# Kernel tuning notes

Measured on AMD Instinct MI355X. Metric: run time of the kernel, lower is better.

## Reference

```python
import jax, jax.numpy as jnp
import numpy as np

B, T, F = 8192, 336, 8
H = 20        # lstm_hidden_size
DENSE = 20
OUT = 1
N_LAYERS = 3


def _param(key, shape, scale):
    return jax.random.uniform(key, shape, jnp.float32, -scale, scale)


def setup_inputs() -> dict:
    key = jax.random.key(0)
    ks = jax.random.split(key, 32)
    s = 1.0 / np.sqrt(H)
    inp = {"x": jax.random.normal(ks[0], (B, T, F), jnp.float32)}
    k = 1
    for l in range(N_LAYERS):
        in_size = F if l == 0 else H
        inp[f"W_ih{l}"] = _param(ks[k], (4 * H, in_size), s); k += 1
        inp[f"W_hh{l}"] = _param(ks[k], (4 * H, H), s); k += 1
        inp[f"b_ih{l}"] = _param(ks[k], (4 * H,), s); k += 1
        inp[f"b_hh{l}"] = _param(ks[k], (4 * H,), s); k += 1
    inp["fc1_w"] = _param(ks[k], (DENSE, H), 1.0 / np.sqrt(H)); k += 1
    inp["fc1_b"] = _param(ks[k], (DENSE,), 1.0 / np.sqrt(H)); k += 1
    inp["fc2_w"] = _param(ks[k], (OUT, DENSE), 1.0 / np.sqrt(DENSE)); k += 1
    inp["fc2_b"] = _param(ks[k], (OUT,), 1.0 / np.sqrt(DENSE)); k += 1
    return inp


def lstm_layer(x, W_ih, W_hh, b_ih, b_hh):
    """PyTorch-convention LSTM over [B, T, in]; returns hidden sequence [B, T, H]."""
    b = x.shape[0]
    # Precompute input contribution for all timesteps in one GEMM: [B, T, 4H]
    xg = jnp.einsum('bti,gi->btg', x, W_ih) + b_ih + b_hh
    W_hh_T = W_hh.T  # [H, 4H]

    def step(carry, xt):
        h, c = carry
        gates = xt + h @ W_hh_T                      # [B, 4H], gate order i,f,g,o
        i, f, g, o = jnp.split(gates, 4, axis=-1)
        i = jax.nn.sigmoid(i)
        f = jax.nn.sigmoid(f)
        g = jnp.tanh(g)
        o = jax.nn.sigmoid(o)
        c = f * c + i * g
        h = o * jnp.tanh(c)
        return (h, c), h

    h0 = jnp.zeros((b, W_hh.shape[1]), x.dtype)
    c0 = jnp.zeros_like(h0)
    _, hs = jax.lax.scan(step, (h0, c0), jnp.swapaxes(xg, 0, 1))  # [T, B, H]
    return jnp.swapaxes(hs, 0, 1)


def reference(x, W_ih0, W_hh0, b_ih0, b_hh0, W_ih1, W_hh1, b_ih1, b_hh1,
              W_ih2, W_hh2, b_ih2, b_hh2, fc1_w, fc1_b, fc2_w, fc2_b):
    layers = [(W_ih0, W_hh0, b_ih0, b_hh0),
              (W_ih1, W_hh1, b_ih1, b_hh1),
              (W_ih2, W_hh2, b_ih2, b_hh2)]
    h = x
    for (wi, wh, bi, bh) in layers:
        h = lstm_layer(h, wi, wh, bi, bh)
    h = h[:, -1, :]                         # last timestep, [B, H]
    # dropout layers are identity at inference
    h = jax.nn.relu(h @ fc1_w.T + fc1_b)    # [B, DENSE]
    return h @ fc2_w.T + fc2_b              # [B, OUT]
```

## Files before the change

### kernel.cpp

```cpp
#include <hip/hip_runtime.h>


#define T_LEN 336
#define NJ 85

typedef _Float16 f16;
typedef _Float16 f16x4 __attribute__((ext_vector_type(4)));
typedef _Float16 f16x8 __attribute__((ext_vector_type(8)));
typedef float f32x4 __attribute__((ext_vector_type(4)));
typedef int i32x2 __attribute__((ext_vector_type(2)));
typedef int i32x4 __attribute__((ext_vector_type(4)));

#define MFMA(a, b, c) __builtin_amdgcn_mfma_f32_16x16x32_f16((a), (b), (c), 0, 0, 0)

#define SWZ1(n, c) ((c) ^ (((n) & 7) << 3))

#define KS1 1.4426950408889634f
#define KS2 2.8853900817779268f

__device__ __forceinline__ float sigm_p(float y) {
  return __builtin_amdgcn_rcpf(1.0f + __builtin_amdgcn_exp2f(y));
}
__device__ __forceinline__ float tanh_p(float y) {
  return 2.0f * __builtin_amdgcn_rcpf(1.0f + __builtin_amdgcn_exp2f(y)) - 1.0f;
}
__device__ __forceinline__ float tanh_fast(float x) {
  return 2.0f * __builtin_amdgcn_rcpf(1.0f + __builtin_amdgcn_exp2f(-KS2 * x)) - 1.0f;
}

#define CELLS5(DI, DF, DG, DO, DL, HV, HL) {                                                \
  { float i_=sigm_p((DI)[0]), f_=sigm_p((DF)[0]), g_=tanh_p((DG)[0]), o_=sigm_p((DO)[0]);   \
    c0 = f_*c0 + i_*g_; (HV)[0] = (f16)(o_*tanh_fast(c0)); }                                \
  { float i_=sigm_p((DI)[1]), f_=sigm_p((DF)[1]), g_=tanh_p((DG)[1]), o_=sigm_p((DO)[1]);   \
    c1 = f_*c1 + i_*g_; (HV)[1] = (f16)(o_*tanh_fast(c1)); }                                \
  { float i_=sigm_p((DI)[2]), f_=sigm_p((DF)[2]), g_=tanh_p((DG)[2]), o_=sigm_p((DO)[2]);   \
    c2 = f_*c2 + i_*g_; (HV)[2] = (f16)(o_*tanh_fast(c2)); }                                \
  { float i_=sigm_p((DI)[3]), f_=sigm_p((DF)[3]), g_=tanh_p((DG)[3]), o_=sigm_p((DO)[3]);   \
    c3 = f_*c3 + i_*g_; (HV)[3] = (f16)(o_*tanh_fast(c3)); }                                \
  { float i_=sigm_p((DL)[0]), f_=sigm_p((DL)[1]), g_=tanh_p((DL)[2]), o_=sigm_p((DL)[3]);   \
    cL = f_*cL + i_*g_; (HL) = (f16)(o_*tanh_fast(cL)); } }

#define MSTEP_REG(BA, PUB) {                                                                \
  i32x2 _lo = __builtin_bit_cast(i32x2, hvS);                                               \
  int _hlu = (int)(unsigned)__builtin_bit_cast(unsigned short, hlS);                        \
  int _b0 = __builtin_amdgcn_ds_bpermute(adrA, _lo.x);                                      \
  int _b1 = __builtin_amdgcn_ds_bpermute(adrA, _lo.y);                                      \
  int _b2 = __builtin_amdgcn_ds_bpermute(adrB, _lo.x);                                      \
  int _b3 = __builtin_amdgcn_ds_bpermute(adrB, _lo.y);                                      \
  int _hA = __builtin_amdgcn_ds_bpermute(adr0, _hlu);                                       \
  int _hB = __builtin_amdgcn_ds_bpermute(adr1, _hlu);                                       \
  int _hC = __builtin_amdgcn_ds_bpermute(adr2, _hlu);                                       \
  int _hD = __builtin_amdgcn_ds_bpermute(adr3, _hlu);                                       \
  int _w0 = (q < 2) ? _b0 : ((_hA & 0xffff) | (_hB << 16));                                 \
  int _w1 = (q < 2) ? _b1 : ((_hC & 0xffff) | (_hD << 16));                                 \
  i32x4 _bbi = { _w0, _w1, _b2, _b3 };                                                      \
  f16x8 bb = __builtin_bit_cast(f16x8, _bbi);                                               \
  f32x4 di = MFMA(Fb0, bb, MFMA(Fa0, (BA), Bi));                                            \
  f32x4 df = MFMA(Fb1, bb, MFMA(Fa1, (BA), Bf));                                            \
  f32x4 dg = MFMA(Fb2, bb, MFMA(Fa2, (BA), Bg));                                            \
  f32x4 dn = MFMA(Fb3, bb, MFMA(Fa3, (BA), Bo));                                            \
  f32x4 dl = MFMA(Fb4, bb, MFMA(Fa4, (BA), BL));                                            \
  f16x4 hv; f16 hl; CELLS5(di, df, dg, dn, dl, hv, hl)                                      \
  hvS = hv; hlS = hl;                                                                       \
  f16* dp_ = (PUB);                                                                         \
  if (dp_) { *(f16x4*)&dp_[n * 64 + SWZ1(n, q * 4)] = hv;                                   \
             dp_[n * 64 + SWZ1(n, 16 + q)] = hl; } }

#define L0S(S, D, PUB) {                                                                    \
  f16x8 b0 = *(const f16x8*)&zT0[S][n * 64 + SWZ1(n, q * 8)];                               \
  f32x4 di = MFMA(Fa0, b0, Bi), df = MFMA(Fa1, b0, Bf), dg = MFMA(Fa2, b0, Bg),             \
        dn = MFMA(Fa3, b0, Bo), dl = MFMA(Fa4, b0, BL);                                     \
  f16x4 hv; f16 hl; CELLS5(di, df, dg, dn, dl, hv, hl)                                      \
  *(f16x4*)&zT0[D][n * 64 + SWZ1(n, 8 + q * 4)] = hv;                                       \
  zT0[D][n * 64 + SWZ1(n, 24 + q)] = hl;                                                    \
  f16* dp_ = (PUB);                                                                         \
  *(f16x4*)&dp_[n * 64 + SWZ1(n, q * 4)] = hv;                                              \
  dp_[n * 64 + SWZ1(n, 16 + q)] = hl; }

__global__ __launch_bounds__(192, 2) void lstm3_ws_kernel(
    const float* __restrict__ x,
    const float* __restrict__ Wih0, const float* __restrict__ Whh0,
    const float* __restrict__ bih0, const float* __restrict__ bhh0,
    const float* __restrict__ Wih1, const float* __restrict__ Whh1,
    const float* __restrict__ bih1, const float* __restrict__ bhh1,
    const float* __restrict__ Wih2, const float* __restrict__ Whh2,
    const float* __restrict__ bih2, const float* __restrict__ bhh2,
    const float* __restrict__ fc1w, const float* __restrict__ fc1b,
    const float* __restrict__ fc2w, const float* __restrict__ fc2b,
    float* __restrict__ out)
{
  __shared__ __align__(16) f16 zT0[4][16 * 64];
  __shared__ __align__(16) f16 zT1[2][4][16 * 64];
  __shared__ __align__(16) f16 zT2[2][4][16 * 64];
  __shared__ __align__(16) float pbuf[64];

  const int tid  = threadIdx.x;
  const int w    = tid >> 6;
  const int lane = tid & 63;
  const int n = lane & 15;
  const int q = lane >> 4;

  const int adrA = 4 * (n + 32 * (q & 1));
  const int adrB = 4 * (n + 16 + 32 * (q & 1));
  const int adr0 = 4 * n, adr1 = 4 * (n + 16), adr2 = 4 * (n + 32), adr3 = 4 * (n + 48);

  {
    f16x8 zer;
#pragma unroll
    for (int j = 0; j < 8; ++j) zer[j] = (f16)0.f;
    for (int i = tid; i < 512; i += 192)  ((f16x8*)&zT0[0][0])[i] = zer;
    for (int i = tid; i < 1024; i += 192) ((f16x8*)&zT1[0][0][0])[i] = zer;
    for (int i = tid; i < 1024; i += 192) ((f16x8*)&zT2[0][0][0])[i] = zer;
  }
  __syncthreads();

  auto rowmap = [](int T, int m) { return T < 4 ? T * 20 + m : (m & 3) * 20 + 16 + (m >> 2); };
  auto gscale = [](int T, int m) {
    int g = (T < 4) ? T : (m & 3);
    return (g == 2) ? -KS2 : -KS1;
  };

  f16x8 Fa0{}, Fa1{}, Fa2{}, Fa3{}, Fa4{};
  f16x8 Fb0{}, Fb1{}, Fb2{}, Fb3{}, Fb4{};
  f32x4 Bi{}, Bf{}, Bg{}, Bo{}, BL{};
  float c0 = 0.f, c1 = 0.f, c2 = 0.f, c3 = 0.f, cL = 0.f;
  f16x4 hvS{};
  f16 hlS = (f16)0.f;

  if (w == 0) {
    auto gA0 = [&](int T) {
      int row = rowmap(T, n);
      float sc = gscale(T, n);
      f16x8 r;
#pragma unroll
      for (int j = 0; j < 8; ++j) {
        int k = q * 8 + j;
        float v = (k < 8) ? Wih0[row * 8 + k] : (k < 28 ? Whh0[row * 20 + k - 8] : 0.f);
        r[j] = (f16)(sc * v);
      }
      return r;
    };
    Fa0 = gA0(0); Fa1 = gA0(1); Fa2 = gA0(2); Fa3 = gA0(3); Fa4 = gA0(4);
    auto gB = [&](int T) {
      f32x4 r;
#pragma unroll
      for (int j = 0; j < 4; ++j) {
        int m = q * 4 + j;
        int row = rowmap(T, m);
        r[j] = gscale(T, m) * (bih0[row] + bhh0[row]);
      }
      return r;
    };
    Bi = gB(0); Bf = gB(1); Bg = gB(2); Bo = gB(3); BL = gB(4);
  } else {
    const float* Wi = (w == 1) ? Wih1 : Wih2;
    const float* Wh = (w == 1) ? Whh1 : Whh2;
    const float* bi = (w == 1) ? bih1 : bih2;
    const float* bh = (w == 1) ? bhh1 : bhh2;
    auto gA = [&](int T, int c) {
      int row = rowmap(T, n);
      float sc = gscale(T, n);
      const float* W = c ? Wh : Wi;
      f16x8 r;
#pragma unroll
      for (int j = 0; j < 8; ++j) {
        int k = q * 8 + j;
        r[j] = (f16)((k < 20) ? sc * W[row * 20 + k] : 0.f);
      }
      return r;
    };
    Fa0 = gA(0, 0); Fb0 = gA(0, 1);
    Fa1 = gA(1, 0); Fb1 = gA(1, 1);
    Fa2 = gA(2, 0); Fb2 = gA(2, 1);
    Fa3 = gA(3, 0); Fb3 = gA(3, 1);
    Fa4 = gA(4, 0); Fb4 = gA(4, 1);
    auto gB = [&](int T) {
      f32x4 r;
#pragma unroll
      for (int j = 0; j < 4; ++j) {
        int m = q * 4 + j;
        int row = rowmap(T, m);
        r[j] = gscale(T, m) * (bi[row] + bh[row]);
      }
      return r;
    };
    Bi = gB(0); Bf = gB(1); Bg = gB(2); Bo = gB(3); BL = gB(4);
  }

  const float* xb = x + (size_t)(blockIdx.x * 16 + n) * (T_LEN * 8) + 4 * q;
  f32x4 xA{}, xB{};
  if (w == 0) {
    xA = *(const f32x4*)(xb);
    xB = *(const f32x4*)(xb + 16);
  }

#pragma unroll 1
  for (int j = 0; j <= NJ; ++j) {
    asm volatile("" ::: "memory");
    __builtin_amdgcn_s_setprio(1);
    const int wp = j & 1, rp = wp ^ 1;
    if (w == 0) {
      if (j <= 83) {
        f16x4 xh;
        xh[0] = (f16)xA[0]; xh[1] = (f16)xA[1]; xh[2] = (f16)xA[2]; xh[3] = (f16)xA[3];
        *(f16x4*)&zT0[q >> 1][n * 64 + SWZ1(n, 4 * (q & 1))] = xh;
        xh[0] = (f16)xB[0]; xh[1] = (f16)xB[1]; xh[2] = (f16)xB[2]; xh[3] = (f16)xB[3];
        *(f16x4*)&zT0[2 + (q >> 1)][n * 64 + SWZ1(n, 4 * (q & 1))] = xh;
        int g = (j + 1 > 83) ? 83 : j + 1;
        xA = *(const f32x4*)(xb + (size_t)(2 * g) * 16);
        xB = *(const f32x4*)(xb + (size_t)(2 * g + 1) * 16);
        f16* p1 = &zT1[wp][0][0];
        L0S(0, 1, p1 + 0 * 1024)
        L0S(1, 2, p1 + 1 * 1024)
        L0S(2, 3, p1 + 2 * 1024)
        L0S(3, 0, p1 + 3 * 1024)
      }
    } else if (w == 1) {
      if (j >= 1 && j <= 84) {
        f16* s1 = &zT1[rp][0][0];
        f16x8 ba0 = *(const f16x8*)&s1[0 * 1024 + n * 64 + SWZ1(n, q * 8)];
        f16x8 ba1 = *(const f16x8*)&s1[1 * 1024 + n * 64 + SWZ1(n, q * 8)];
        f16x8 ba2 = *(const f16x8*)&s1[2 * 1024 + n * 64 + SWZ1(n, q * 8)];
        f16x8 ba3 = *(const f16x8*)&s1[3 * 1024 + n * 64 + SWZ1(n, q * 8)];
        f16* p2 = &zT2[wp][0][0];
        MSTEP_REG(ba0, p2 + 0 * 1024)
        MSTEP_REG(ba1, p2 + 1 * 1024)
        MSTEP_REG(ba2, p2 + 2 * 1024)
        MSTEP_REG(ba3, p2 + 3 * 1024)
      }
    } else {
      if (j >= 2) {
        f16* s2 = &zT2[rp][0][0];
        f16x8 ca0 = *(const f16x8*)&s2[0 * 1024 + n * 64 + SWZ1(n, q * 8)];
        f16x8 ca1 = *(const f16x8*)&s2[1 * 1024 + n * 64 + SWZ1(n, q * 8)];
        f16x8 ca2 = *(const f16x8*)&s2[2 * 1024 + n * 64 + SWZ1(n, q * 8)];
        f16x8 ca3 = *(const f16x8*)&s2[3 * 1024 + n * 64 + SWZ1(n, q * 8)];
        MSTEP_REG(ca0, (f16*)nullptr)
        MSTEP_REG(ca1, (f16*)nullptr)
        MSTEP_REG(ca2, (f16*)nullptr)
        MSTEP_REG(ca3, (f16*)nullptr)
      }
    }
    __builtin_amdgcn_s_setprio(0);
    asm volatile("s_waitcnt lgkmcnt(0)\n\ts_barrier" ::: "memory");
  }

  if (w == 2) {
    *(f16x4*)&zT2[1][0][n * 64 + SWZ1(n, 32 + q * 4)] = hvS;
    zT2[1][0][n * 64 + SWZ1(n, 48 + q)] = hlS;
    asm volatile("s_waitcnt lgkmcnt(0)" ::: "memory");
    const f16* hb = &zT2[1][0][0];
    f16x4 hv0 = *(const f16x4*)&hb[n * 64 + SWZ1(n, 32)];
    f16x4 hv1 = *(const f16x4*)&hb[n * 64 + SWZ1(n, 36)];
    f16x4 hv2 = *(const f16x4*)&hb[n * 64 + SWZ1(n, 40)];
    f16x4 hv3 = *(const f16x4*)&hb[n * 64 + SWZ1(n, 44)];
    f16x4 hv4 = *(const f16x4*)&hb[n * 64 + SWZ1(n, 48)];
    float p = 0.f;
#pragma unroll
    for (int i = 0; i < 5; ++i) {
      int d = q * 5 + i;
      const float* wr = fc1w + d * 20;
      float s = fc1b[d]
        + wr[0]  * (float)hv0[0] + wr[1]  * (float)hv0[1] + wr[2]  * (float)hv0[2] + wr[3]  * (float)hv0[3]
        + wr[4]  * (float)hv1[0] + wr[5]  * (float)hv1[1] + wr[6]  * (float)hv1[2] + wr[7]  * (float)hv1[3]
        + wr[8]  * (float)hv2[0] + wr[9]  * (float)hv2[1] + wr[10] * (float)hv2[2] + wr[11] * (float)hv2[3]
        + wr[12] * (float)hv3[0] + wr[13] * (float)hv3[1] + wr[14] * (float)hv3[2] + wr[15] * (float)hv3[3]
        + wr[16] * (float)hv4[0] + wr[17] * (float)hv4[1] + wr[18] * (float)hv4[2] + wr[19] * (float)hv4[3];
      p += fc2w[d] * fmaxf(s, 0.f);
    }
    pbuf[n * 4 + q] = p;
    if (q == 0) {
      f32x4 pv = *(const f32x4*)&pbuf[n * 4];
      out[blockIdx.x * 16 + n] = pv[0] + pv[1] + pv[2] + pv[3] + fc2b[0];
    }
  }
}

extern "C" void kernel_launch(void* const* d_in, const int* in_sizes, int n_in,
                              void* d_out, int out_size, void* d_ws, size_t ws_size,
                              hipStream_t stream) {
  const float* x    = (const float*)d_in[0];
  const float* Wih0 = (const float*)d_in[1];
  const float* Whh0 = (const float*)d_in[2];
  const float* bih0 = (const float*)d_in[3];
  const float* bhh0 = (const float*)d_in[4];
  const float* Wih1 = (const float*)d_in[5];
  const float* Whh1 = (const float*)d_in[6];
  const float* bih1 = (const float*)d_in[7];
  const float* bhh1 = (const float*)d_in[8];
  const float* Wih2 = (const float*)d_in[9];
  const float* Whh2 = (const float*)d_in[10];
  const float* bih2 = (const float*)d_in[11];
  const float* bhh2 = (const float*)d_in[12];
  const float* fc1w = (const float*)d_in[13];
  const float* fc1b = (const float*)d_in[14];
  const float* fc2w = (const float*)d_in[15];
  const float* fc2b = (const float*)d_in[16];
  float* out = (float*)d_out;

  hipLaunchKernelGGL(lstm3_ws_kernel, dim3(8192 / 16), dim3(192), 0, stream,
                     x, Wih0, Whh0, bih0, bhh0,
                     Wih1, Whh1, bih1, bhh1,
                     Wih2, Whh2, bih2, bhh2,
                     fc1w, fc1b, fc2w, fc2b, out);
}
```

Before: 387.5 us.

## Process two interleaved 16-row batch tiles per wave to hide recurrence latency

Each block now handles 32 batch rows as two independent 16-row chains, interleaving their MFMA and cell steps within every wave, so one chain's dependent latency can overlap the other's work. Launch bounds drop to one block per SM hint, the grid is halved, and LDS buffers are doubled, with an unused pad array added to shrink occupancy. The gain relies on instruction-level parallelism replacing wave-level parallelism. The costs are higher register pressure and fewer resident blocks, and the grid falls to 256 blocks, which may underfill the device.

```diff
diff --git a/kernel.cpp b/kernel.cpp
--- a/kernel.cpp
+++ b/kernel.cpp
@@ -28,21 +28,21 @@
   return 2.0f * __builtin_amdgcn_rcpf(1.0f + __builtin_amdgcn_exp2f(-KS2 * x)) - 1.0f;
 }
 
-#define CELLS5(DI, DF, DG, DO, DL, HV, HL) {                                                \
+#define CELLS5(DI, DF, DG, DO, DL, C0, C1, C2, C3, C4, HV, HL) {                            \
   { float i_=sigm_p((DI)[0]), f_=sigm_p((DF)[0]), g_=tanh_p((DG)[0]), o_=sigm_p((DO)[0]);   \
-    c0 = f_*c0 + i_*g_; (HV)[0] = (f16)(o_*tanh_fast(c0)); }                                \
+    C0 = f_*C0 + i_*g_; (HV)[0] = (f16)(o_*tanh_fast(C0)); }                                \
   { float i_=sigm_p((DI)[1]), f_=sigm_p((DF)[1]), g_=tanh_p((DG)[1]), o_=sigm_p((DO)[1]);   \
-    c1 = f_*c1 + i_*g_; (HV)[1] = (f16)(o_*tanh_fast(c1)); }                                \
+    C1 = f_*C1 + i_*g_; (HV)[1] = (f16)(o_*tanh_fast(C1)); }                                \
   { float i_=sigm_p((DI)[2]), f_=sigm_p((DF)[2]), g_=tanh_p((DG)[2]), o_=sigm_p((DO)[2]);   \
-    c2 = f_*c2 + i_*g_; (HV)[2] = (f16)(o_*tanh_fast(c2)); }                                \
+    C2 = f_*C2 + i_*g_; (HV)[2] = (f16)(o_*tanh_fast(C2)); }                                \
   { float i_=sigm_p((DI)[3]), f_=sigm_p((DF)[3]), g_=tanh_p((DG)[3]), o_=sigm_p((DO)[3]);   \
-    c3 = f_*c3 + i_*g_; (HV)[3] = (f16)(o_*tanh_fast(c3)); }                                \
+    C3 = f_*C3 + i_*g_; (HV)[3] = (f16)(o_*tanh_fast(C3)); }                                \
   { float i_=sigm_p((DL)[0]), f_=sigm_p((DL)[1]), g_=tanh_p((DL)[2]), o_=sigm_p((DL)[3]);   \
-    cL = f_*cL + i_*g_; (HL) = (f16)(o_*tanh_fast(cL)); } }
-
-#define MSTEP_REG(BA, PUB) {                                                                \
-  i32x2 _lo = __builtin_bit_cast(i32x2, hvS);                                               \
-  int _hlu = (int)(unsigned)__builtin_bit_cast(unsigned short, hlS);                        \
+    C4 = f_*C4 + i_*g_; (HL) = (f16)(o_*tanh_fast(C4)); } }
+
+#define MSTEP_REG(BA, PUB, HVS, HLS, C0, C1, C2, C3, C4) {                                  \
+  i32x2 _lo = __builtin_bit_cast(i32x2, HVS);                                               \
+  int _hlu = (int)(unsigned)__builtin_bit_cast(unsigned short, HLS);                        \
   int _b0 = __builtin_amdgcn_ds_bpermute(adrA, _lo.x);                                      \
   int _b1 = __builtin_amdgcn_ds_bpermute(adrA, _lo.y);                                      \
   int _b2 = __builtin_amdgcn_ds_bpermute(adrB, _lo.x);                                      \
@@ -60,24 +60,24 @@
   f32x4 dg = MFMA(Fb2, bb, MFMA(Fa2, (BA), Bg));                                            \
   f32x4 dn = MFMA(Fb3, bb, MFMA(Fa3, (BA), Bo));                                            \
   f32x4 dl = MFMA(Fb4, bb, MFMA(Fa4, (BA), BL));                                            \
-  f16x4 hv; f16 hl; CELLS5(di, df, dg, dn, dl, hv, hl)                                      \
-  hvS = hv; hlS = hl;                                                                       \
+  f16x4 hv; f16 hl; CELLS5(di, df, dg, dn, dl, C0, C1, C2, C3, C4, hv, hl)                  \
+  HVS = hv; HLS = hl;                                                                       \
   f16* dp_ = (PUB);                                                                         \
   if (dp_) { *(f16x4*)&dp_[n * 64 + SWZ1(n, q * 4)] = hv;                                   \
              dp_[n * 64 + SWZ1(n, 16 + q)] = hl; } }
 
-#define L0S(S, D, PUB) {                                                                    \
-  f16x8 b0 = *(const f16x8*)&zT0[S][n * 64 + SWZ1(n, q * 8)];                               \
-  f32x4 di = MFMA(Fa0, b0, Bi), df = MFMA(Fa1, b0, Bf), dg = MFMA(Fa2, b0, Bg),             \
-        dn = MFMA(Fa3, b0, Bo), dl = MFMA(Fa4, b0, BL);                                     \
-  f16x4 hv; f16 hl; CELLS5(di, df, dg, dn, dl, hv, hl)                                      \
-  *(f16x4*)&zT0[D][n * 64 + SWZ1(n, 8 + q * 4)] = hv;                                       \
-  zT0[D][n * 64 + SWZ1(n, 24 + q)] = hl;                                                    \
+#define L0S(ZB, S, D, PUB, C0, C1, C2, C3, C4) {                                            \
+  f16x8 _bv = *(const f16x8*)&(ZB)[(S) * 1024 + n * 64 + SWZ1(n, q * 8)];                   \
+  f32x4 di = MFMA(Fa0, _bv, Bi), df = MFMA(Fa1, _bv, Bf), dg = MFMA(Fa2, _bv, Bg),          \
+        dn = MFMA(Fa3, _bv, Bo), dl = MFMA(Fa4, _bv, BL);                                   \
+  f16x4 hv; f16 hl; CELLS5(di, df, dg, dn, dl, C0, C1, C2, C3, C4, hv, hl)                  \
+  *(f16x4*)&(ZB)[(D) * 1024 + n * 64 + SWZ1(n, 8 + q * 4)] = hv;                            \
+  (ZB)[(D) * 1024 + n * 64 + SWZ1(n, 24 + q)] = hl;                                         \
   f16* dp_ = (PUB);                                                                         \
   *(f16x4*)&dp_[n * 64 + SWZ1(n, q * 4)] = hv;                                              \
   dp_[n * 64 + SWZ1(n, 16 + q)] = hl; }
 
-__global__ __launch_bounds__(192, 2) void lstm3_ws_kernel(
+__global__ __launch_bounds__(192, 1) void lstm3_ws_kernel(
     const float* __restrict__ x,
     const float* __restrict__ Wih0, const float* __restrict__ Whh0,
     const float* __restrict__ bih0, const float* __restrict__ bhh0,
@@ -89,10 +89,11 @@
     const float* __restrict__ fc2w, const float* __restrict__ fc2b,
     float* __restrict__ out)
 {
-  __shared__ __align__(16) f16 zT0[4][16 * 64];
-  __shared__ __align__(16) f16 zT1[2][4][16 * 64];
-  __shared__ __align__(16) f16 zT2[2][4][16 * 64];
-  __shared__ __align__(16) float pbuf[64];
+  __shared__ __align__(16) f16 zT0[2][4][1024];
+  __shared__ __align__(16) f16 zT1[2][2][4][1024];
+  __shared__ __align__(16) f16 zT2[2][2][4][1024];
+  __shared__ __align__(16) float pbuf[128];
+  __shared__ __align__(16) f16 lpad[512];
 
   const int tid  = threadIdx.x;
   const int w    = tid >> 6;
@@ -100,6 +101,8 @@
   const int n = lane & 15;
   const int q = lane >> 4;
 
+  if ((int)blockIdx.x < 0) lpad[0] = (f16)1.f;
+
   const int adrA = 4 * (n + 32 * (q & 1));
   const int adrB = 4 * (n + 16 + 32 * (q & 1));
   const int adr0 = 4 * n, adr1 = 4 * (n + 16), adr2 = 4 * (n + 32), adr3 = 4 * (n + 48);
@@ -108,9 +111,9 @@
     f16x8 zer;
 #pragma unroll
     for (int j = 0; j < 8; ++j) zer[j] = (f16)0.f;
-    for (int i = tid; i < 512; i += 192)  ((f16x8*)&zT0[0][0])[i] = zer;
-    for (int i = tid; i < 1024; i += 192) ((f16x8*)&zT1[0][0][0])[i] = zer;
-    for (int i = tid; i < 1024; i += 192) ((f16x8*)&zT2[0][0][0])[i] = zer;
+    for (int i = tid; i < 1024; i += 192) ((f16x8*)&zT0[0][0][0])[i] = zer;
+    for (int i = tid; i < 2048; i += 192) ((f16x8*)&zT1[0][0][0][0])[i] = zer;
+    for (int i = tid; i < 2048; i += 192) ((f16x8*)&zT2[0][0][0][0])[i] = zer;
   }
   __syncthreads();
 
@@ -123,9 +126,10 @@
   f16x8 Fa0{}, Fa1{}, Fa2{}, Fa3{}, Fa4{};
   f16x8 Fb0{}, Fb1{}, Fb2{}, Fb3{}, Fb4{};
   f32x4 Bi{}, Bf{}, Bg{}, Bo{}, BL{};
-  float c0 = 0.f, c1 = 0.f, c2 = 0.f, c3 = 0.f, cL = 0.f;
-  f16x4 hvS{};
-  f16 hlS = (f16)0.f;
+  float cA0 = 0.f, cA1 = 0.f, cA2 = 0.f, cA3 = 0.f, cA4 = 0.f;
+  float cB0 = 0.f, cB1 = 0.f, cB2 = 0.f, cB3 = 0.f, cB4 = 0.f;
+  f16x4 hvA{}, hvB{};
+  f16 hlA = (f16)0.f, hlB = (f16)0.f;
 
   if (w == 0) {
     auto gA0 = [&](int T) {
@@ -187,11 +191,12 @@
     Bi = gB(0); Bf = gB(1); Bg = gB(2); Bo = gB(3); BL = gB(4);
   }
 
-  const float* xb = x + (size_t)(blockIdx.x * 16 + n) * (T_LEN * 8) + 4 * q;
-  f32x4 xA{}, xB{};
+  const float* xb0 = x + (size_t)(blockIdx.x * 32 + n) * (T_LEN * 8) + 4 * q;
+  const float* xb1 = xb0 + (size_t)16 * (T_LEN * 8);
+  f32x4 xA0{}, xB0{}, xA1{}, xB1{};
   if (w == 0) {
-    xA = *(const f32x4*)(xb);
-    xB = *(const f32x4*)(xb + 16);
+    xA0 = *(const f32x4*)(xb0);       xB0 = *(const f32x4*)(xb0 + 16);
+    xA1 = *(const f32x4*)(xb1);       xB1 = *(const f32x4*)(xb1 + 16);
   }
 
 #pragma unroll 1
@@ -202,43 +207,75 @@
     if (w == 0) {
       if (j <= 83) {
         f16x4 xh;
-        xh[0] = (f16)xA[0]; xh[1] = (f16)xA[1]; xh[2] = (f16)xA[2]; xh[3] = (f16)xA[3];
-        *(f16x4*)&zT0[q >> 1][n * 64 + SWZ1(n, 4 * (q & 1))] = xh;
-        xh[0] = (f16)xB[0]; xh[1] = (f16)xB[1]; xh[2] = (f16)xB[2]; xh[3] = (f16)xB[3];
-        *(f16x4*)&zT0[2 + (q >> 1)][n * 64 + SWZ1(n, 4 * (q & 1))] = xh;
+        xh[0] = (f16)xA0[0]; xh[1] = (f16)xA0[1]; xh[2] = (f16)xA0[2]; xh[3] = (f16)xA0[3];
+        *(f16x4*)&zT0[0][q >> 1][n * 64 + SWZ1(n, 4 * (q & 1))] = xh;
+        xh[0] = (f16)xB0[0]; xh[1] = (f16)xB0[1]; xh[2] = (f16)xB0[2]; xh[3] = (f16)xB0[3];
+        *(f16x4*)&zT0[0][2 + (q >> 1)][n * 64 + SWZ1(n, 4 * (q & 1))] = xh;
+        xh[0] = (f16)xA1[0]; xh[1] = (f16)xA1[1]; xh[2] = (f16)xA1[2]; xh[3] = (f16)xA1[3];
+        *(f16x4*)&zT0[1][q >> 1][n * 64 + SWZ1(n, 4 * (q & 1))] = xh;
+        xh[0] = (f16)xB1[0]; xh[1] = (f16)xB1[1]; xh[2] = (f16)xB1[2]; xh[3] = (f16)xB1[3];
+        *(f16x4*)&zT0[1][2 + (q >> 1)][n * 64 + SWZ1(n, 4 * (q & 1))] = xh;
         int g = (j + 1 > 83) ? 83 : j + 1;
-        xA = *(const f32x4*)(xb + (size_t)(2 * g) * 16);
-        xB = *(const f32x4*)(xb + (size_t)(2 * g + 1) * 16);
-        f16* p1 = &zT1[wp][0][0];
-        L0S(0, 1, p1 + 0 * 1024)
-        L0S(1, 2, p1 + 1 * 1024)
-        L0S(2, 3, p1 + 2 * 1024)
-        L0S(3, 0, p1 + 3 * 1024)
+        xA0 = *(const f32x4*)(xb0 + (size_t)(2 * g) * 16);
+        xB0 = *(const f32x4*)(xb0 + (size_t)(2 * g + 1) * 16);
+        xA1 = *(const f32x4*)(xb1 + (size_t)(2 * g) * 16);
+        xB1 = *(const f32x4*)(xb1 + (size_t)(2 * g + 1) * 16);
+        f16* p10 = &zT1[0][wp][0][0];
+        f16* p11 = &zT1[1][wp][0][0];
+        f16* z00 = &zT0[0][0][0];
+        f16* z01 = &zT0[1][0][0];
+        L0S(z00, 0, 1, p10 + 0 * 1024, cA0, cA1, cA2, cA3, cA4)
+        L0S(z01, 0, 1, p11 + 0 * 1024, cB0, cB1, cB2, cB3, cB4)
+        L0S(z00, 1, 2, p10 + 1 * 1024, cA0, cA1, cA2, cA3, cA4)
+        L0S(z01, 1, 2, p11 + 1 * 1024, cB0, cB1, cB2, cB3, cB4)
+        L0S(z00, 2, 3, p10 + 2 * 1024, cA0, cA1, cA2, cA3, cA4)
+        L0S(z01, 2, 3, p11 + 2 * 1024, cB0, cB1, cB2, cB3, cB4)
+        L0S(z00, 3, 0, p10 + 3 * 1024, cA0, cA1, cA2, cA3, cA4)
+        L0S(z01, 3, 0, p11 + 3 * 1024, cB0, cB1, cB2, cB3, cB4)
       }
     } else if (w == 1) {
       if (j >= 1 && j <= 84) {
-        f16* s1 = &zT1[rp][0][0];
-        f16x8 ba0 = *(const f16x8*)&s1[0 * 1024 + n * 64 + SWZ1(n, q * 8)];
-        f16x8 ba1 = *(const f16x8*)&s1[1 * 1024 + n * 64 + SWZ1(n, q * 8)];
-        f16x8 ba2 = *(const f16x8*)&s1[2 * 1024 + n * 64 + SWZ1(n, q * 8)];
-        f16x8 ba3 = *(const f16x8*)&s1[3 * 1024 + n * 64 + SWZ1(n, q * 8)];
-        f16* p2 = &zT2[wp][0][0];
-        MSTEP_REG(ba0, p2 + 0 * 1024)
-        MSTEP_REG(ba1, p2 + 1 * 1024)
-        MSTEP_REG(ba2, p2 + 2 * 1024)
-        MSTEP_REG(ba3, p2 + 3 * 1024)
+        f16* s10 = &zT1[0][rp][0][0];
+        f16* s11 = &zT1[1][rp][0][0];
+        f16x8 a00 = *(const f16x8*)&s10[0 * 1024 + n * 64 + SWZ1(n, q * 8)];
+        f16x8 a01 = *(const f16x8*)&s10[1 * 1024 + n * 64 + SWZ1(n, q * 8)];
+        f16x8 a02 = *(const f16x8*)&s10[2 * 1024 + n * 64 + SWZ1(n, q * 8)];
+        f16x8 a03 = *(const f16x8*)&s10[3 * 1024 + n * 64 + SWZ1(n, q * 8)];
+        f16x8 a10 = *(const f16x8*)&s11[0 * 1024 + n * 64 + SWZ1(n, q * 8)];
+        f16x8 a11 = *(const f16x8*)&s11[1 * 1024 + n * 64 + SWZ1(n, q * 8)];
+        f16x8 a12 = *(const f16x8*)&s11[2 * 1024 + n * 64 + SWZ1(n, q * 8)];
+        f16x8 a13 = *(const f16x8*)&s11[3 * 1024 + n * 64 + SWZ1(n, q * 8)];
+        f16* p20 = &zT2[0][wp][0][0];
+        f16* p21 = &zT2[1][wp][0][0];
+        MSTEP_REG(a00, p20 + 0 * 1024, hvA, hlA, cA0, cA1, cA2, cA3, cA4)
+        MSTEP_REG(a10, p21 + 0 * 1024, hvB, hlB, cB0, cB1, cB2, cB3, cB4)
+        MSTEP_REG(a01, p20 + 1 * 1024, hvA, hlA, cA0, cA1, cA2, cA3, cA4)
+        MSTEP_REG(a11, p21 + 1 * 1024, hvB, hlB, cB0, cB1, cB2, cB3, cB4)
+        MSTEP_REG(a02, p20 + 2 * 1024, hvA, hlA, cA0, cA1, cA2, cA3, cA4)
+        MSTEP_REG(a12, p21 + 2 * 1024, hvB, hlB, cB0, cB1, cB2, cB3, cB4)
+        MSTEP_REG(a03, p20 + 3 * 1024, hvA, hlA, cA0, cA1, cA2, cA3, cA4)
+        MSTEP_REG(a13, p21 + 3 * 1024, hvB, hlB, cB0, cB1, cB2, cB3, cB4)
       }
     } else {
       if (j >= 2) {
-        f16* s2 = &zT2[rp][0][0];
-        f16x8 ca0 = *(const f16x8*)&s2[0 * 1024 + n * 64 + SWZ1(n, q * 8)];
-        f16x8 ca1 = *(const f16x8*)&s2[1 * 1024 + n * 64 + SWZ1(n, q * 8)];
-        f16x8 ca2 = *(const f16x8*)&s2[2 * 1024 + n * 64 + SWZ1(n, q * 8)];
-        f16x8 ca3 = *(const f16x8*)&s2[3 * 1024 + n * 64 + SWZ1(n, q * 8)];
-        MSTEP_REG(ca0, (f16*)nullptr)
-        MSTEP_REG(ca1, (f16*)nullptr)
-        MSTEP_REG(ca2, (f16*)nullptr)
-        MSTEP_REG(ca3, (f16*)nullptr)
+        f16* s20 = &zT2[0][rp][0][0];
+        f16* s21 = &zT2[1][rp][0][0];
+        f16x8 a00 = *(const f16x8*)&s20[0 * 1024 + n * 64 + SWZ1(n, q * 8)];
+        f16x8 a01 = *(const f16x8*)&s20[1 * 1024 + n * 64 + SWZ1(n, q * 8)];
+        f16x8 a02 = *(const f16x8*)&s20[2 * 1024 + n * 64 + SWZ1(n, q * 8)];
+        f16x8 a03 = *(const f16x8*)&s20[3 * 1024 + n * 64 + SWZ1(n, q * 8)];
+        f16x8 a10 = *(const f16x8*)&s21[0 * 1024 + n * 64 + SWZ1(n, q * 8)];
+        f16x8 a11 = *(const f16x8*)&s21[1 * 1024 + n * 64 + SWZ1(n, q * 8)];
+        f16x8 a12 = *(const f16x8*)&s21[2 * 1024 + n * 64 + SWZ1(n, q * 8)];
+        f16x8 a13 = *(const f16x8*)&s21[3 * 1024 + n * 64 + SWZ1(n, q * 8)];
+        MSTEP_REG(a00, (f16*)nullptr, hvA, hlA, cA0, cA1, cA2, cA3, cA4)
+        MSTEP_REG(a10, (f16*)nullptr, hvB, hlB, cB0, cB1, cB2, cB3, cB4)
+        MSTEP_REG(a01, (f16*)nullptr, hvA, hlA, cA0, cA1, cA2, cA3, cA4)
+        MSTEP_REG(a11, (f16*)nullptr, hvB, hlB, cB0, cB1, cB2, cB3, cB4)
+        MSTEP_REG(a02, (f16*)nullptr, hvA, hlA, cA0, cA1, cA2, cA3, cA4)
+        MSTEP_REG(a12, (f16*)nullptr, hvB, hlB, cB0, cB1, cB2, cB3, cB4)
+        MSTEP_REG(a03, (f16*)nullptr, hvA, hlA, cA0, cA1, cA2, cA3, cA4)
+        MSTEP_REG(a13, (f16*)nullptr, hvB, hlB, cB0, cB1, cB2, cB3, cB4)
       }
     }
     __builtin_amdgcn_s_setprio(0);
@@ -246,32 +283,37 @@
   }
 
   if (w == 2) {
-    *(f16x4*)&zT2[1][0][n * 64 + SWZ1(n, 32 + q * 4)] = hvS;
-    zT2[1][0][n * 64 + SWZ1(n, 48 + q)] = hlS;
+    *(f16x4*)&zT2[0][1][0][n * 64 + SWZ1(n, 32 + q * 4)] = hvA;
+    zT2[0][1][0][n * 64 + SWZ1(n, 48 + q)] = hlA;
+    *(f16x4*)&zT2[1][1][0][n * 64 + SWZ1(n, 32 + q * 4)] = hvB;
+    zT2[1][1][0][n * 64 + SWZ1(n, 48 + q)] = hlB;
     asm volatile("s_waitcnt lgkmcnt(0)" ::: "memory");
-    const f16* hb = &zT2[1][0][0];
-    f16x4 hv0 = *(const f16x4*)&hb[n * 64 + SWZ1(n, 32)];
-    f16x4 hv1 = *(const f16x4*)&hb[n * 64 + SWZ1(n, 36)];
-    f16x4 hv2 = *(const f16x4*)&hb[n * 64 + SWZ1(n, 40)];
-    f16x4 hv3 = *(const f16x4*)&hb[n * 64 + SWZ1(n, 44)];
-    f16x4 hv4 = *(const f16x4*)&hb[n * 64 + SWZ1(n, 48)];
-    float p = 0.f;
-#pragma unroll
-    for (int i = 0; i < 5; ++i) {
-      int d = q * 5 + i;
-      const float* wr = fc1w + d * 20;
-      float s = fc1b[d]
-        + wr[0]  * (float)hv0[0] + wr[1]  * (float)hv0[1] + wr[2]  * (float)hv0[2] + wr[3]  * (float)hv0[3]
-        + wr[4]  * (float)hv1[0] + wr[5]  * (float)hv1[1] + wr[6]  * (float)hv1[2] + wr[7]  * (float)hv1[3]
-        + wr[8]  * (float)hv2[0] + wr[9]  * (float)hv2[1] + wr[10] * (float)hv2[2] + wr[11] * (float)hv2[3]
-        + wr[12] * (float)hv3[0] + wr[13] * (float)hv3[1] + wr[14] * (float)hv3[2] + wr[15] * (float)hv3[3]
-        + wr[16] * (float)hv4[0] + wr[17] * (float)hv4[1] + wr[18] * (float)hv4[2] + wr[19] * (float)hv4[3];
-      p += fc2w[d] * fmaxf(s, 0.f);
-    }
-    pbuf[n * 4 + q] = p;
-    if (q == 0) {
-      f32x4 pv = *(const f32x4*)&pbuf[n * 4];
-      out[blockIdx.x * 16 + n] = pv[0] + pv[1] + pv[2] + pv[3] + fc2b[0];
+#pragma unroll
+    for (int u = 0; u < 2; ++u) {
+      const f16* hb = u ? &zT2[1][1][0][0] : &zT2[0][1][0][0];
+      f16x4 hv0 = *(const f16x4*)&hb[n * 64 + SWZ1(n, 32)];
+      f16x4 hv1 = *(const f16x4*)&hb[n * 64 + SWZ1(n, 36)];
+      f16x4 hv2 = *(const f16x4*)&hb[n * 64 + SWZ1(n, 40)];
+      f16x4 hv3 = *(const f16x4*)&hb[n * 64 + SWZ1(n, 44)];
+      f16x4 hv4 = *(const f16x4*)&hb[n * 64 + SWZ1(n, 48)];
+      float p = 0.f;
+#pragma unroll
+      for (int i = 0; i < 5; ++i) {
+        int d = q * 5 + i;
+        const float* wr = fc1w + d * 20;
+        float s = fc1b[d]
+          + wr[0]  * (float)hv0[0] + wr[1]  * (float)hv0[1] + wr[2]  * (float)hv0[2] + wr[3]  * (float)hv0[3]
+          + wr[4]  * (float)hv1[0] + wr[5]  * (float)hv1[1] + wr[6]  * (float)hv1[2] + wr[7]  * (float)hv1[3]
+          + wr[8]  * (float)hv2[0] + wr[9]  * (float)hv2[1] + wr[10] * (float)hv2[2] + wr[11] * (float)hv2[3]
+          + wr[12] * (float)hv3[0] + wr[13] * (float)hv3[1] + wr[14] * (float)hv3[2] + wr[15] * (float)hv3[3]
+          + wr[16] * (float)hv4[0] + wr[17] * (float)hv4[1] + wr[18] * (float)hv4[2] + wr[19] * (float)hv4[3];
+        p += fc2w[d] * fmaxf(s, 0.f);
+      }
+      pbuf[u * 64 + n * 4 + q] = p;
+      if (q == 0) {
+        f32x4 pv = *(const f32x4*)&pbuf[u * 64 + n * 4];
+        out[blockIdx.x * 32 + u * 16 + n] = pv[0] + pv[1] + pv[2] + pv[3] + fc2b[0];
+      }
     }
   }
 }
@@ -298,7 +340,7 @@
   const float* fc2b = (const float*)d_in[16];
   float* out = (float*)d_out;
 
-  hipLaunchKernelGGL(lstm3_ws_kernel, dim3(8192 / 16), dim3(192), 0, stream,
+  hipLaunchKernelGGL(lstm3_ws_kernel, dim3(8192 / 32), dim3(192), 0, stream,
                      x, Wih0, Whh0, bih0, bhh0,
                      Wih1, Whh1, bih1, bhh1,
                      Wih2, Whh2, bih2, bhh2,
```

After: 434.6 us. 12.2% more time.

## Process eight timesteps per barrier interval instead of four in wavefront LSTM pipeline

Applied to the files above, without the earlier changes.

The warp-specialized three-layer pipeline now handles eight timesteps per stage per iteration. Two timesteps are packed into each 64-column shared-memory row at column offsets 0 and 32. This halves the number of outer iterations and block-wide barriers (NJ 85 to 43) and doubles the x prefetch depth. The cost is more live registers per wave and a longer pipeline fill and drain, since each stage now lags by eight steps.

```diff
diff --git a/kernel.cpp b/kernel.cpp
--- a/kernel.cpp
+++ b/kernel.cpp
@@ -2,7 +2,7 @@
 
 
 #define T_LEN 336
-#define NJ 85
+#define NJ 43
 
 typedef _Float16 f16;
 typedef _Float16 f16x4 __attribute__((ext_vector_type(4)));
@@ -40,7 +40,7 @@
   { float i_=sigm_p((DL)[0]), f_=sigm_p((DL)[1]), g_=tanh_p((DL)[2]), o_=sigm_p((DL)[3]);   \
     cL = f_*cL + i_*g_; (HL) = (f16)(o_*tanh_fast(cL)); } }
 
-#define MSTEP_REG(BA, PUB) {                                                                \
+#define MSTEP_REG(BA, PUB, PC) {                                                            \
   i32x2 _lo = __builtin_bit_cast(i32x2, hvS);                                               \
   int _hlu = (int)(unsigned)__builtin_bit_cast(unsigned short, hlS);                        \
   int _b0 = __builtin_amdgcn_ds_bpermute(adrA, _lo.x);                                      \
@@ -63,19 +63,19 @@
   f16x4 hv; f16 hl; CELLS5(di, df, dg, dn, dl, hv, hl)                                      \
   hvS = hv; hlS = hl;                                                                       \
   f16* dp_ = (PUB);                                                                         \
-  if (dp_) { *(f16x4*)&dp_[n * 64 + SWZ1(n, q * 4)] = hv;                                   \
-             dp_[n * 64 + SWZ1(n, 16 + q)] = hl; } }
-
-#define L0S(S, D, PUB) {                                                                    \
-  f16x8 b0 = *(const f16x8*)&zT0[S][n * 64 + SWZ1(n, q * 8)];                               \
+  if (dp_) { *(f16x4*)&dp_[n * 64 + SWZ1(n, (PC) + q * 4)] = hv;                            \
+             dp_[n * 64 + SWZ1(n, (PC) + 16 + q)] = hl; } }
+
+#define L0S(SR, SC, DR, DC, PUBP, PC) {                                                     \
+  f16x8 b0 = *(const f16x8*)&zT0[SR][n * 64 + SWZ1(n, (SC) + q * 8)];                       \
   f32x4 di = MFMA(Fa0, b0, Bi), df = MFMA(Fa1, b0, Bf), dg = MFMA(Fa2, b0, Bg),             \
         dn = MFMA(Fa3, b0, Bo), dl = MFMA(Fa4, b0, BL);                                     \
   f16x4 hv; f16 hl; CELLS5(di, df, dg, dn, dl, hv, hl)                                      \
-  *(f16x4*)&zT0[D][n * 64 + SWZ1(n, 8 + q * 4)] = hv;                                       \
-  zT0[D][n * 64 + SWZ1(n, 24 + q)] = hl;                                                    \
-  f16* dp_ = (PUB);                                                                         \
-  *(f16x4*)&dp_[n * 64 + SWZ1(n, q * 4)] = hv;                                              \
-  dp_[n * 64 + SWZ1(n, 16 + q)] = hl; }
+  *(f16x4*)&zT0[DR][n * 64 + SWZ1(n, (DC) + 8 + q * 4)] = hv;                               \
+  zT0[DR][n * 64 + SWZ1(n, (DC) + 24 + q)] = hl;                                            \
+  f16* dp_ = (PUBP);                                                                        \
+  *(f16x4*)&dp_[n * 64 + SWZ1(n, (PC) + q * 4)] = hv;                                       \
+  dp_[n * 64 + SWZ1(n, (PC) + 16 + q)] = hl; }
 
 __global__ __launch_bounds__(192, 2) void lstm3_ws_kernel(
     const float* __restrict__ x,
@@ -89,9 +89,9 @@
     const float* __restrict__ fc2w, const float* __restrict__ fc2b,
     float* __restrict__ out)
 {
-  __shared__ __align__(16) f16 zT0[4][16 * 64];
-  __shared__ __align__(16) f16 zT1[2][4][16 * 64];
-  __shared__ __align__(16) f16 zT2[2][4][16 * 64];
+  __shared__ __align__(16) f16 zT0[4][1024];
+  __shared__ __align__(16) f16 zT1[2][4][1024];
+  __shared__ __align__(16) f16 zT2[2][4][1024];
   __shared__ __align__(16) float pbuf[64];
 
   const int tid  = threadIdx.x;
@@ -188,10 +188,12 @@
   }
 
   const float* xb = x + (size_t)(blockIdx.x * 16 + n) * (T_LEN * 8) + 4 * q;
-  f32x4 xA{}, xB{};
+  f32x4 xA{}, xB{}, xC{}, xD{};
   if (w == 0) {
     xA = *(const f32x4*)(xb);
     xB = *(const f32x4*)(xb + 16);
+    xC = *(const f32x4*)(xb + 32);
+    xD = *(const f32x4*)(xb + 48);
   }
 
 #pragma unroll 1
@@ -200,45 +202,71 @@
     __builtin_amdgcn_s_setprio(1);
     const int wp = j & 1, rp = wp ^ 1;
     if (w == 0) {
-      if (j <= 83) {
+      if (j <= 41) {
         f16x4 xh;
         xh[0] = (f16)xA[0]; xh[1] = (f16)xA[1]; xh[2] = (f16)xA[2]; xh[3] = (f16)xA[3];
-        *(f16x4*)&zT0[q >> 1][n * 64 + SWZ1(n, 4 * (q & 1))] = xh;
+        *(f16x4*)&zT0[0][n * 64 + SWZ1(n, (q >> 1) * 32 + 4 * (q & 1))] = xh;
         xh[0] = (f16)xB[0]; xh[1] = (f16)xB[1]; xh[2] = (f16)xB[2]; xh[3] = (f16)xB[3];
-        *(f16x4*)&zT0[2 + (q >> 1)][n * 64 + SWZ1(n, 4 * (q & 1))] = xh;
-        int g = (j + 1 > 83) ? 83 : j + 1;
-        xA = *(const f32x4*)(xb + (size_t)(2 * g) * 16);
-        xB = *(const f32x4*)(xb + (size_t)(2 * g + 1) * 16);
+        *(f16x4*)&zT0[1][n * 64 + SWZ1(n, (q >> 1) * 32 + 4 * (q & 1))] = xh;
+        xh[0] = (f16)xC[0]; xh[1] = (f16)xC[1]; xh[2] = (f16)xC[2]; xh[3] = (f16)xC[3];
+        *(f16x4*)&zT0[2][n * 64 + SWZ1(n, (q >> 1) * 32 + 4 * (q & 1))] = xh;
+        xh[0] = (f16)xD[0]; xh[1] = (f16)xD[1]; xh[2] = (f16)xD[2]; xh[3] = (f16)xD[3];
+        *(f16x4*)&zT0[3][n * 64 + SWZ1(n, (q >> 1) * 32 + 4 * (q & 1))] = xh;
+        int g = (j + 1 > 41) ? 41 : j + 1;
+        xA = *(const f32x4*)(xb + (size_t)(4 * g) * 16);
+        xB = *(const f32x4*)(xb + (size_t)(4 * g + 1) * 16);
+        xC = *(const f32x4*)(xb + (size_t)(4 * g + 2) * 16);
+        xD = *(const f32x4*)(xb + (size_t)(4 * g + 3) * 16);
         f16* p1 = &zT1[wp][0][0];
-        L0S(0, 1, p1 + 0 * 1024)
-        L0S(1, 2, p1 + 1 * 1024)
-        L0S(2, 3, p1 + 2 * 1024)
-        L0S(3, 0, p1 + 3 * 1024)
+        L0S(0, 0,  0, 32, p1 + 0 * 1024, 0)
+        L0S(0, 32, 1, 0,  p1 + 0 * 1024, 32)
+        L0S(1, 0,  1, 32, p1 + 1 * 1024, 0)
+        L0S(1, 32, 2, 0,  p1 + 1 * 1024, 32)
+        L0S(2, 0,  2, 32, p1 + 2 * 1024, 0)
+        L0S(2, 32, 3, 0,  p1 + 2 * 1024, 32)
+        L0S(3, 0,  3, 32, p1 + 3 * 1024, 0)
+        L0S(3, 32, 0, 0,  p1 + 3 * 1024, 32)
       }
     } else if (w == 1) {
-      if (j >= 1 && j <= 84) {
+      if (j >= 1 && j <= 42) {
         f16* s1 = &zT1[rp][0][0];
-        f16x8 ba0 = *(const f16x8*)&s1[0 * 1024 + n * 64 + SWZ1(n, q * 8)];
-        f16x8 ba1 = *(const f16x8*)&s1[1 * 1024 + n * 64 + SWZ1(n, q * 8)];
-        f16x8 ba2 = *(const f16x8*)&s1[2 * 1024 + n * 64 + SWZ1(n, q * 8)];
-        f16x8 ba3 = *(const f16x8*)&s1[3 * 1024 + n * 64 + SWZ1(n, q * 8)];
+        f16x8 a0 = *(const f16x8*)&s1[0 * 1024 + n * 64 + SWZ1(n, 0  + q * 8)];
+        f16x8 a1 = *(const f16x8*)&s1[0 * 1024 + n * 64 + SWZ1(n, 32 + q * 8)];
+        f16x8 a2 = *(const f16x8*)&s1[1 * 1024 + n * 64 + SWZ1(n, 0  + q * 8)];
+        f16x8 a3 = *(const f16x8*)&s1[1 * 1024 + n * 64 + SWZ1(n, 32 + q * 8)];
+        f16x8 a4 = *(const f16x8*)&s1[2 * 1024 + n * 64 + SWZ1(n, 0  + q * 8)];
+        f16x8 a5 = *(const f16x8*)&s1[2 * 1024 + n * 64 + SWZ1(n, 32 + q * 8)];
+        f16x8 a6 = *(const f16x8*)&s1[3 * 1024 + n * 64 + SWZ1(n, 0  + q * 8)];
+        f16x8 a7 = *(const f16x8*)&s1[3 * 1024 + n * 64 + SWZ1(n, 32 + q * 8)];
         f16* p2 = &zT2[wp][0][0];
-        MSTEP_REG(ba0, p2 + 0 * 1024)
-        MSTEP_REG(ba1, p2 + 1 * 1024)
-        MSTEP_REG(ba2, p2 + 2 * 1024)
-        MSTEP_REG(ba3, p2 + 3 * 1024)
+        MSTEP_REG(a0, p2 + 0 * 1024, 0)
+        MSTEP_REG(a1, p2 + 0 * 1024, 32)
+        MSTEP_REG(a2, p2 + 1 * 1024, 0)
+        MSTEP_REG(a3, p2 + 1 * 1024, 32)
+        MSTEP_REG(a4, p2 + 2 * 1024, 0)
+        MSTEP_REG(a5, p2 + 2 * 1024, 32)
+        MSTEP_REG(a6, p2 + 3 * 1024, 0)
+        MSTEP_REG(a7, p2 + 3 * 1024, 32)
       }
     } else {
       if (j >= 2) {
         f16* s2 = &zT2[rp][0][0];
-        f16x8 ca0 = *(const f16x8*)&s2[0 * 1024 + n * 64 + SWZ1(n, q * 8)];
-        f16x8 ca1 = *(const f16x8*)&s2[1 * 1024 + n * 64 + SWZ1(n, q * 8)];
-        f16x8 ca2 = *(const f16x8*)&s2[2 * 1024 + n * 64 + SWZ1(n, q * 8)];
-        f16x8 ca3 = *(const f16x8*)&s2[3 * 1024 + n * 64 + SWZ1(n, q * 8)];
-        MSTEP_REG(ca0, (f16*)nullptr)
-        MSTEP_REG(ca1, (f16*)nullptr)
-        MSTEP_REG(ca2, (f16*)nullptr)
-        MSTEP_REG(ca3, (f16*)nullptr)
+        f16x8 a0 = *(const f16x8*)&s2[0 * 1024 + n * 64 + SWZ1(n, 0  + q * 8)];
+        f16x8 a1 = *(const f16x8*)&s2[0 * 1024 + n * 64 + SWZ1(n, 32 + q * 8)];
+        f16x8 a2 = *(const f16x8*)&s2[1 * 1024 + n * 64 + SWZ1(n, 0  + q * 8)];
+        f16x8 a3 = *(const f16x8*)&s2[1 * 1024 + n * 64 + SWZ1(n, 32 + q * 8)];
+        f16x8 a4 = *(const f16x8*)&s2[2 * 1024 + n * 64 + SWZ1(n, 0  + q * 8)];
+        f16x8 a5 = *(const f16x8*)&s2[2 * 1024 + n * 64 + SWZ1(n, 32 + q * 8)];
+        f16x8 a6 = *(const f16x8*)&s2[3 * 1024 + n * 64 + SWZ1(n, 0  + q * 8)];
+        f16x8 a7 = *(const f16x8*)&s2[3 * 1024 + n * 64 + SWZ1(n, 32 + q * 8)];
+        MSTEP_REG(a0, (f16*)nullptr, 0)
+        MSTEP_REG(a1, (f16*)nullptr, 0)
+        MSTEP_REG(a2, (f16*)nullptr, 0)
+        MSTEP_REG(a3, (f16*)nullptr, 0)
+        MSTEP_REG(a4, (f16*)nullptr, 0)
+        MSTEP_REG(a5, (f16*)nullptr, 0)
+        MSTEP_REG(a6, (f16*)nullptr, 0)
+        MSTEP_REG(a7, (f16*)nullptr, 0)
       }
     }
     __builtin_amdgcn_s_setprio(0);
```

Result: no change. 386.2 us (-0.3%).
